# Kernel optimization log

Measured on AMD Instinct MI355X. Metric: run time of the kernel, lower is better.

Reference implementation:

```python
import jax, jax.numpy as jnp
import numpy as np

_N = 2048          # matrix_size (A_sparse.shape[0] in the original)
_NNZ = 32768       # number of factor / pred entries
_LOGCOND_EPS = 1e-12


def setup_inputs() -> dict:
    key = jax.random.key(0)
    k1, k2, k3, k4, k5 = jax.random.split(key, 5)
    pred_values = jax.random.normal(k1, (_NNZ,), dtype=jnp.float32)
    active_scales = jax.random.uniform(k2, (_NNZ,), dtype=jnp.float32) * 0.05
    A_factor = jax.random.normal(k3, (_N, _N), dtype=jnp.float32)
    factor_rows = jax.random.randint(k4, (_NNZ,), 0, _N, dtype=jnp.int32)
    factor_cols = jax.random.randint(k5, (_NNZ,), 0, _N, dtype=jnp.int32)
    return {
        "pred_values": pred_values,
        "active_scales": active_scales,
        "A_factor": A_factor,
        "factor_rows": factor_rows,
        "factor_cols": factor_cols,
    }


def reference(pred_values, active_scales, A_factor, factor_rows, factor_cols):
    n = A_factor.shape[0]
    dt = pred_values.dtype
    # SPD system matrix A (stands in for the original fixed A_sparse)
    A = A_factor @ A_factor.T / jnp.asarray(n, dt) + jnp.eye(n, dtype=dt)
    # Sparse factor L assembled from predicted values (scatter-add, dup-safe),
    # unit diagonal keeps L A L^T well conditioned / SPD.
    L = jnp.eye(n, dtype=dt).at[factor_rows, factor_cols].add(pred_values * active_scales)
    # Preconditioned matrix M = L A L^T (symmetric PSD)
    M = L @ A @ L.T
    M = 0.5 * (M + M.T)
    evals = jnp.linalg.eigvalsh(M)  # ascending
    lam_min = jnp.maximum(evals[0], _LOGCOND_EPS)
    lam_max = jnp.maximum(evals[-1], _LOGCOND_EPS)
    # loss = log(lambda_max) - log(lambda_min) = log condition number
    return jnp.log(lam_max) - jnp.log(lam_min)
```

## Files before the change

kernel.cpp:

```cpp
#include <hip/hip_runtime.h>

#define N2 2048
#define NNZ 32768
#define LK 22
#define NBL 128
#define BINCAP 64

typedef __attribute__((ext_vector_type(8))) _Float16 half8;
typedef __attribute__((ext_vector_type(4))) float f32x4;

#define AGENT __HIP_MEMORY_SCOPE_AGENT
#define AS1C(p) ((const __attribute__((address_space(1))) unsigned int*)(p))
#define AS3(p)  ((__attribute__((address_space(3))) unsigned int*)(p))

__device__ __forceinline__ unsigned short f2h(float f) {
  _Float16 h = (_Float16)f;
  return *(unsigned short*)&h;
}
__device__ __forceinline__ float h2f(unsigned short u) {
  _Float16 h = *(_Float16*)&u;
  return (float)h;
}

__global__ __launch_bounds__(256) void convert_kernel(const float* __restrict__ W,
                                                      unsigned short* __restrict__ Hf,
                                                      unsigned* __restrict__ cnt) {
  if (blockIdx.x < 8) cnt[blockIdx.x * 256 + threadIdx.x] = 0;
  int i4 = blockIdx.x * 256 + threadIdx.x;
  float4 w = ((const float4*)W)[i4];
  ushort4 h;
  h.x = f2h(w.x); h.y = f2h(w.y); h.z = f2h(w.z); h.w = f2h(w.w);
  ((ushort4*)Hf)[i4] = h;
}

__global__ __launch_bounds__(512) void gemm_f16_kernel(const unsigned short* __restrict__ Hf,
                                                       unsigned short* __restrict__ Ah,
                                                       const float* __restrict__ pred,
                                                       const float* __restrict__ scal,
                                                       const int* __restrict__ rows,
                                                       const int* __restrict__ cols,
                                                       unsigned* __restrict__ cnt,
                                                       int* __restrict__ bcol,
                                                       float* __restrict__ bval) {
  const int tid = threadIdx.x;
  if (blockIdx.x < 64) {
    int k = blockIdx.x * 512 + tid;
    int r = rows[k];
    unsigned pos = atomicAdd(&cnt[r], 1u);
    if (pos < BINCAP) {
      bcol[r * BINCAP + pos] = cols[k];
      bval[r * BINCAP + pos] = pred[k] * scal[k];
    }
  }

  __shared__ unsigned short Xs[2][64 * 32];
  __shared__ unsigned short Ys[2][128 * 32];
  __shared__ float Cred[64 * 132];
  const int w = tid >> 6, lane = tid & 63;
  const int half = w >> 2, wq = w & 3;
  const int swz = ((blockIdx.x & 7) << 6) | (blockIdx.x >> 3);
  const int bi = swz >> 4, bj = swz & 15;
  const int row0 = bi * 64, col0 = bj * 128;
  const int m0 = (wq & 1) * 32, n0 = (wq >> 1) * 64;
  f32x4 acc[2][4];
#pragma unroll
  for (int a = 0; a < 2; ++a)
#pragma unroll
    for (int b = 0; b < 4; ++b) acc[a][b] = (f32x4){0.f, 0.f, 0.f, 0.f};
  const int mrow = lane & 15, kseg = (lane >> 4) * 8;
  const int srowX = wq * 16 + (lane >> 2);
  const int srowY = wq * 32 + (lane >> 2);
  const int scol = (lane & 3) * 8;
  const int kbase = half * 1024;

  for (int k0 = 0; k0 < 1024; k0 += 32) {
    __syncthreads();
    __builtin_amdgcn_global_load_lds(
        AS1C(Hf + (size_t)(row0 + srowX) * 2048 + kbase + k0 + scol),
        AS3(Xs[half] + (wq * 16) * 32), 16, 0, 0);
#pragma unroll
    for (int q = 0; q < 2; ++q) {
      __builtin_amdgcn_global_load_lds(
          AS1C(Hf + (size_t)(col0 + srowY + q * 16) * 2048 + kbase + k0 + scol),
          AS3(Ys[half] + (wq * 32 + q * 16) * 32), 16, 0, 0);
    }
    __syncthreads();
    half8 af[2], bf[4];
#pragma unroll
    for (int t = 0; t < 2; ++t)
      af[t] = *(const half8*)(Xs[half] + (m0 + t * 16 + mrow) * 32 + kseg);
#pragma unroll
    for (int t = 0; t < 4; ++t)
      bf[t] = *(const half8*)(Ys[half] + (n0 + t * 16 + mrow) * 32 + kseg);
#pragma unroll
    for (int mt = 0; mt < 2; ++mt)
#pragma unroll
      for (int nt = 0; nt < 4; ++nt)
        acc[mt][nt] = __builtin_amdgcn_mfma_f32_16x16x32_f16(af[mt], bf[nt], acc[mt][nt], 0, 0, 0);
  }
  const int crow = (lane >> 4) * 4, ccol = lane & 15;
  __syncthreads();
  if (half == 1) {
#pragma unroll
    for (int mt = 0; mt < 2; ++mt)
#pragma unroll
      for (int nt = 0; nt < 4; ++nt)
#pragma unroll
        for (int r = 0; r < 4; ++r)
          Cred[(m0 + mt * 16 + crow + r) * 132 + n0 + nt * 16 + ccol] = acc[mt][nt][r];
  }
  __syncthreads();
  if (half == 0) {
    const float invn = 1.0f / 2048.0f;
#pragma unroll
    for (int mt = 0; mt < 2; ++mt)
#pragma unroll
      for (int nt = 0; nt < 4; ++nt) {
        const int gi0 = row0 + m0 + mt * 16 + crow;
        const int gj = col0 + n0 + nt * 16 + ccol;
        size_t base = (size_t)gi0 * 2048 + gj;
#pragma unroll
        for (int r = 0; r < 4; ++r) {
          float v = acc[mt][nt][r] +
                    Cred[(m0 + mt * 16 + crow + r) * 132 + n0 + nt * 16 + ccol];
          Ah[base + (size_t)r * 2048] = f2h(v * invn + ((gi0 + r == gj) ? 1.0f : 0.0f));
        }
      }
  }
}

__global__ __launch_bounds__(256) void gatherF_kernel(const unsigned* __restrict__ cnt,
                                                      const int* __restrict__ bcol,
                                                      const float* __restrict__ bval,
                                                      const unsigned short* __restrict__ Ah,
                                                      unsigned short* __restrict__ F) {
  const int r = blockIdx.x, tid = threadIdx.x;
  __shared__ int scol_[BINCAP];
  __shared__ float sval_[BINCAP];
  const unsigned ne = min(cnt[r], (unsigned)BINCAP);
  if (tid < ne) {
    scol_[tid] = bcol[r * BINCAP + tid];
    sval_[tid] = bval[r * BINCAP + tid];
  }
  __syncthreads();
  float acc[8] = {0.f, 0.f, 0.f, 0.f, 0.f, 0.f, 0.f, 0.f};
  unsigned e = 0;
  for (; e + 4 <= ne; e += 4) {
    uint4 q0 = *(const uint4*)(Ah + (size_t)scol_[e + 0] * 2048 + tid * 8);
    uint4 q1 = *(const uint4*)(Ah + (size_t)scol_[e + 1] * 2048 + tid * 8);
    uint4 q2 = *(const uint4*)(Ah + (size_t)scol_[e + 2] * 2048 + tid * 8);
    uint4 q3 = *(const uint4*)(Ah + (size_t)scol_[e + 3] * 2048 + tid * 8);
    half8 h0 = *(half8*)&q0, h1 = *(half8*)&q1, h2 = *(half8*)&q2, h3 = *(half8*)&q3;
    const float v0 = sval_[e], v1 = sval_[e + 1], v2 = sval_[e + 2], v3 = sval_[e + 3];
#pragma unroll
    for (int k = 0; k < 8; ++k) {
      acc[k] += v0 * (float)h0[k];
      acc[k] += v1 * (float)h1[k];
      acc[k] += v2 * (float)h2[k];
      acc[k] += v3 * (float)h3[k];
    }
  }
  for (; e < ne; ++e) {
    uint4 q = *(const uint4*)(Ah + (size_t)scol_[e] * 2048 + tid * 8);
    half8 hv = *(half8*)&q;
    const float v = sval_[e];
#pragma unroll
    for (int k = 0; k < 8; ++k) acc[k] += v * (float)hv[k];
  }
  unsigned short o[8];
#pragma unroll
  for (int k = 0; k < 8; ++k) o[k] = f2h(acc[k]);
  *(uint4*)(F + (size_t)r * 2048 + tid * 8) = *(uint4*)o;
}

__global__ __launch_bounds__(256) void transpose_kernel(const unsigned short* __restrict__ F,
                                                        unsigned short* __restrict__ Ft) {
  __shared__ unsigned short T2[64][66];
  const int bi = blockIdx.x, bj = blockIdx.y;
  const int c8 = (threadIdx.x & 7) * 8;
  const int rr = threadIdx.x >> 3;
#pragma unroll
  for (int h = 0; h < 2; ++h) {
    const int r = rr + h * 32;
    uint4 raw = *(const uint4*)(F + (size_t)(bj * 64 + r) * 2048 + bi * 64 + c8);
    const unsigned* pw = (const unsigned*)&raw;
#pragma unroll
    for (int i = 0; i < 4; ++i)
      *(unsigned*)&T2[r][c8 + i * 2] = pw[i];
  }
  __syncthreads();
#pragma unroll
  for (int h = 0; h < 2; ++h) {
    const int r = rr + h * 32;
    unsigned short tv[8];
#pragma unroll
    for (int k = 0; k < 8; ++k) tv[k] = T2[c8 + k][r];
    *(uint4*)(Ft + (size_t)(bi * 64 + r) * 2048 + bj * 64 + c8) = *(uint4*)tv;
  }
}

__global__ __launch_bounds__(256) void finalM_kernel(const unsigned* __restrict__ cnt,
                                                     const int* __restrict__ bcol,
                                                     const float* __restrict__ bval,
                                                     const unsigned short* __restrict__ Ah,
                                                     const unsigned short* __restrict__ F,
                                                     const unsigned short* __restrict__ Ft,
                                                     float* __restrict__ M) {
  const int r = blockIdx.x, tid = threadIdx.x;
  __shared__ int scol_[BINCAP];
  __shared__ float sval_[BINCAP];
  const unsigned ne = min(cnt[r], (unsigned)BINCAP);
  if (tid < ne) {
    scol_[tid] = bcol[r * BINCAP + tid];
    sval_[tid] = bval[r * BINCAP + tid];
  }
  __syncthreads();
  float acc[8] = {0.f, 0.f, 0.f, 0.f, 0.f, 0.f, 0.f, 0.f};
  unsigned e = 0;
  for (; e + 4 <= ne; e += 4) {
    uint4 q0 = *(const uint4*)(Ft + (size_t)scol_[e + 0] * 2048 + tid * 8);
    uint4 q1 = *(const uint4*)(Ft + (size_t)scol_[e + 1] * 2048 + tid * 8);
    uint4 q2 = *(const uint4*)(Ft + (size_t)scol_[e + 2] * 2048 + tid * 8);
    uint4 q3 = *(const uint4*)(Ft + (size_t)scol_[e + 3] * 2048 + tid * 8);
    half8 h0 = *(half8*)&q0, h1 = *(half8*)&q1, h2 = *(half8*)&q2, h3 = *(half8*)&q3;
    const float v0 = sval_[e], v1 = sval_[e + 1], v2 = sval_[e + 2], v3 = sval_[e + 3];
#pragma unroll
    for (int k = 0; k < 8; ++k) {
      acc[k] += v0 * (float)h0[k];
      acc[k] += v1 * (float)h1[k];
      acc[k] += v2 * (float)h2[k];
      acc[k] += v3 * (float)h3[k];
    }
  }
  for (; e < ne; ++e) {
    uint4 q = *(const uint4*)(Ft + (size_t)scol_[e] * 2048 + tid * 8);
    half8 hv = *(half8*)&q;
    const float v = sval_[e];
#pragma unroll
    for (int k = 0; k < 8; ++k) acc[k] += v * (float)hv[k];
  }
  const size_t off = (size_t)r * 2048 + tid * 8;
  uint4 ra = *(const uint4*)(Ah + off);
  uint4 rf = *(const uint4*)(F + off);
  uint4 rt = *(const uint4*)(Ft + off);
  half8 ha = *(half8*)&ra, hf = *(half8*)&rf, ht = *(half8*)&rt;
  float out[8];
#pragma unroll
  for (int k = 0; k < 8; ++k)
    out[k] = (float)ha[k] + ((float)hf[k] + (float)ht[k]) + acc[k];
  float4* Mo = (float4*)(M + off);
  Mo[0] = (float4){out[0], out[1], out[2], out[3]};
  Mo[1] = (float4){out[4], out[5], out[6], out[7]};
}

__device__ __forceinline__ float block_sum8(float v, float* red) {
#pragma unroll
  for (int off = 32; off; off >>= 1) v += __shfl_down(v, off);
  if ((threadIdx.x & 63) == 0) red[threadIdx.x >> 6] = v;
  __syncthreads();
  float r = ((red[0] + red[1]) + (red[2] + red[3])) +
            ((red[4] + red[5]) + (red[6] + red[7]));
  __syncthreads();
  return r;
}

__global__ __launch_bounds__(512) void lanczos_kernel(const float* __restrict__ M,
                                                      unsigned long long* __restrict__ Z0,
                                                      unsigned long long* __restrict__ Z1,
                                                      float* __restrict__ out) {
  const int tid = threadIdx.x, b = blockIdx.x;
  const int wave = tid >> 6, lane = tid & 63;
  __shared__ __align__(16) float Mlds[16 * 2048];
  __shared__ __align__(16) float VA[2048];
  __shared__ __align__(16) float VB[2048];
  __shared__ float red[8];
  __shared__ float al[LK + 2], b2[LK + 2];
  __shared__ float bnds[2], res[2];

  const float* Mblk = M + (size_t)b * 16 * 2048;
#pragma unroll
  for (int q = 0; q < 16; ++q)
    __builtin_amdgcn_global_load_lds(AS1C(Mblk + wave * 4096 + q * 256 + lane * 4),
                                     AS3(Mlds + wave * 4096 + q * 256), 16, 0, 0);

  float pv[4];
  float part = 0.f;
#pragma unroll
  for (int t = 0; t < 4; ++t) {
    int i = t * 512 + tid;
    unsigned u = (unsigned)i * 2654435761u;
    u ^= u >> 16; u *= 2246822519u; u ^= u >> 13;
    float rv = (float)(u >> 8) * (2.f / 16777216.f) - 1.f;
    pv[t] = rv;
    part += rv * rv;
  }
  float nrm = block_sum8(part, red);
  float innm = rsqrtf(nrm);
#pragma unroll
  for (int t = 0; t < 4; ++t) {
    int i = t * 512 + tid;
    VA[i] = pv[t] * innm;
    VB[i] = 0.f;
  }
  __syncthreads();

  float* Vcur = VA;
  float* Vprev = VB;
  float beta_prev = 0.f;

  for (int j = 1; j <= LK; ++j) {
    unsigned long long* Z = (j & 1) ? Z0 : Z1;
#pragma unroll
    for (int rr = 0; rr < 2; ++rr) {
      const int r = b * 16 + wave * 2 + rr;
      const float4* Mr = (const float4*)(Mlds + (wave * 2 + rr) * 2048);
      float s = 0.f;
#pragma unroll
      for (int t = 0; t < 8; ++t) {
        int idx = t * 64 + lane;
        float4 m4 = Mr[idx];
        float4 v4 = ((const float4*)Vcur)[idx];
        s += m4.x * v4.x + m4.y * v4.y + m4.z * v4.z + m4.w * v4.w;
      }
#pragma unroll
      for (int off = 32; off; off >>= 1) s += __shfl_down(s, off);
      if (lane == 0) {
        float zv = s - beta_prev * Vprev[r];
        unsigned long long pk = ((unsigned long long)(unsigned)j << 32) |
                                (unsigned long long)(unsigned)__float_as_uint(zv);
        __hip_atomic_store(&Z[r], pk, __ATOMIC_RELAXED, AGENT);
      }
    }

    float va[4];
#pragma unroll
    for (int t = 0; t < 4; ++t) va[t] = Vcur[t * 512 + tid];

    unsigned long long w4[4];
    int rounds = 0;
    for (;;) {
      bool ok = true;
#pragma unroll
      for (int t = 0; t < 4; ++t) {
        w4[t] = __hip_atomic_load(&Z[t * 512 + tid], __ATOMIC_RELAXED, AGENT);
        ok &= ((unsigned)(w4[t] >> 32) == (unsigned)j);
      }
      if (ok) break;
      if (rounds == 1)      __builtin_amdgcn_s_sleep(1);
      else if (rounds == 2) __builtin_amdgcn_s_sleep(2);
      else if (rounds >= 3) __builtin_amdgcn_s_sleep(8);
      ++rounds;
    }
    float za[4];
    float pa = 0.f;
#pragma unroll
    for (int t = 0; t < 4; ++t) {
      za[t] = __uint_as_float((unsigned)w4[t]);
      pa += za[t] * va[t];
    }
    float alpha = block_sum8(pa, red);
    float pb = 0.f;
#pragma unroll
    for (int t = 0; t < 4; ++t) {
      float rsd = za[t] - alpha * va[t];
      pb += rsd * rsd;
    }
    float beta2 = block_sum8(pb, red);
    float beta = sqrtf(fmaxf(beta2, 1e-30f));
    float invb = 1.f / beta;
    if (tid == 0) { al[j] = alpha; b2[j] = beta2; }
#pragma unroll
    for (int t = 0; t < 4; ++t) {
      int i = t * 512 + tid;
      Vprev[i] = (za[t] - alpha * va[t]) * invb;
    }
    float* tmp = Vprev; Vprev = Vcur; Vcur = tmp;
    beta_prev = beta;
    __syncthreads();
  }

  if (b == 0) {
    if (tid == 0) {
      float lo = 1e30f, hi = -1e30f;
      for (int i = 1; i <= LK; ++i) {
        float bl = (i > 1) ? sqrtf(b2[i - 1]) : 0.f;
        float br = (i < LK) ? sqrtf(b2[i]) : 0.f;
        lo = fminf(lo, al[i] - bl - br);
        hi = fmaxf(hi, al[i] + bl + br);
      }
      bnds[0] = lo; bnds[1] = hi;
    }
    __syncthreads();
    if (wave < 2) {
      const int tcount = (wave == 0) ? 1 : LK;
      float lo = bnds[0], hi = bnds[1];
      for (int round = 0; round < 4; ++round) {
        float x = lo + (hi - lo) * (float)(lane + 1) * (1.f / 65.f);
        int cnt = 0;
        float d = al[1] - x;
        if (fabsf(d) < 1e-25f) d = -1e-25f;
        if (d < 0.f) cnt++;
        for (int i = 2; i <= LK; ++i) {
          d = (al[i] - x) - b2[i - 1] / d;
          if (fabsf(d) < 1e-25f) d = -1e-25f;
          if (d < 0.f) cnt++;
        }
        bool ab = (cnt >= tcount);
        float cand_hi = ab ? x : hi;
        float cand_lo = ab ? lo : x;
#pragma unroll
        for (int off = 32; off; off >>= 1) {
          cand_hi = fminf(cand_hi, __shfl_down(cand_hi, off));
          cand_lo = fmaxf(cand_lo, __shfl_down(cand_lo, off));
        }
        cand_hi = __shfl(cand_hi, 0);
        cand_lo = __shfl(cand_lo, 0);
        hi = cand_hi;
        lo = fminf(cand_lo, hi);
      }
      if (lane == 0) res[wave] = 0.5f * (lo + hi);
    }
    __syncthreads();
    if (tid == 0) {
      float lmin = fmaxf(res[0], 1e-12f);
      float lmax = fmaxf(res[1], 1e-12f);
      out[0] = logf(lmax) - logf(lmin);
    }
  }
}

extern "C" void kernel_launch(void* const* d_in, const int* in_sizes, int n_in,
                              void* d_out, int out_size, void* d_ws, size_t ws_size,
                              hipStream_t stream) {
  const float* pred = (const float*)d_in[0];
  const float* scal = (const float*)d_in[1];
  const float* W    = (const float*)d_in[2];
  const int*   rows = (const int*)d_in[3];
  const int*   cols = (const int*)d_in[4];
  float* out = (float*)d_out;

  char* ws = (char*)d_ws;
  const size_t MB = 1024 * 1024;
  unsigned short* Hf = (unsigned short*)(ws);
  unsigned short* Ah = (unsigned short*)(ws + 8 * MB);
  unsigned short* F  = (unsigned short*)(ws + 16 * MB);
  unsigned short* Ft = (unsigned short*)(ws);
  float* M = (float*)(ws + 24 * MB);
  char* ctrl = ws + 40 * MB;
  unsigned* cnt  = (unsigned*)(ctrl);
  int*      bcol = (int*)(ctrl + 8192);
  float*    bval = (float*)(ctrl + 8192 + 524288);
  unsigned long long* Z0 = (unsigned long long*)(ctrl + 8192 + 1048576);
  unsigned long long* Z1 = (unsigned long long*)(ctrl + 8192 + 1048576 + 16384);

  convert_kernel<<<4096, 256, 0, stream>>>(W, Hf, cnt);
  gemm_f16_kernel<<<512, 512, 0, stream>>>(Hf, Ah, pred, scal, rows, cols, cnt, bcol, bval);

  gatherF_kernel<<<2048, 256, 0, stream>>>(cnt, bcol, bval, Ah, F);
  transpose_kernel<<<dim3(32, 32), 256, 0, stream>>>(F, Ft);
  finalM_kernel<<<2048, 256, 0, stream>>>(cnt, bcol, bval, Ah, F, Ft, M);

  lanczos_kernel<<<NBL, 512, 0, stream>>>(M, Z0, Z1, out);
}
```

Measured before the change: 256.5 us.

## Exploit symmetry of A: compute lower-triangle GEMM tiles and mirror-store transposes

The W·W^T GEMM now launches only the 272 tiles on or below the diagonal (in 128-column block units) instead of all 512. Each off-diagonal tile writes its result and also writes the transposed tile through shared memory, which roughly halves the GEMM arithmetic. The cost is an extra barrier and transposed store per block, fewer blocks to spread across the CUs, and a small serial loop to decode the tile index. The bcol/bval binning in blocks below 64 still runs because the block count stays above 64.

```diff
diff --git a/kernel.cpp b/kernel.cpp
--- a/kernel.cpp
+++ b/kernel.cpp
@@ -53,13 +53,24 @@
     }
   }
 
+  int bi, bj;
+  bool diag;
+  if (blockIdx.x < 32) {
+    bi = blockIdx.x; bj = bi >> 1; diag = true;
+  } else {
+    int idx = blockIdx.x - 32;
+    int j = 0;
+    while (j < 14 && idx >= (j + 1) * (30 - j)) ++j;
+    bj = j;
+    bi = 2 * j + 2 + (idx - j * (31 - j));
+    diag = false;
+  }
+
   __shared__ unsigned short Xs[2][64 * 32];
   __shared__ unsigned short Ys[2][128 * 32];
   __shared__ float Cred[64 * 132];
   const int w = tid >> 6, lane = tid & 63;
   const int half = w >> 2, wq = w & 3;
-  const int swz = ((blockIdx.x & 7) << 6) | (blockIdx.x >> 3);
-  const int bi = swz >> 4, bj = swz & 15;
   const int row0 = bi * 64, col0 = bj * 128;
   const int m0 = (wq & 1) * 32, n0 = (wq >> 1) * 64;
   f32x4 acc[2][4];
@@ -121,11 +132,25 @@
         size_t base = (size_t)gi0 * 2048 + gj;
 #pragma unroll
         for (int r = 0; r < 4; ++r) {
-          float v = acc[mt][nt][r] +
-                    Cred[(m0 + mt * 16 + crow + r) * 132 + n0 + nt * 16 + ccol];
-          Ah[base + (size_t)r * 2048] = f2h(v * invn + ((gi0 + r == gj) ? 1.0f : 0.0f));
+          const int li = (m0 + mt * 16 + crow + r) * 132 + n0 + nt * 16 + ccol;
+          float val = (acc[mt][nt][r] + Cred[li]) * invn +
+                      ((gi0 + r == gj) ? 1.0f : 0.0f);
+          Ah[base + (size_t)r * 2048] = f2h(val);
+          if (!diag) Cred[li] = val;
         }
       }
+  }
+  if (!diag) {
+    __syncthreads();
+    const int orow = tid >> 2;
+    const int cseg = (tid & 3) * 16;
+    unsigned short mv[16];
+#pragma unroll
+    for (int k = 0; k < 16; ++k)
+      mv[k] = f2h(Cred[(cseg + k) * 132 + orow]);
+    uint4* dst = (uint4*)(Ah + (size_t)(col0 + orow) * 2048 + row0 + cseg);
+    dst[0] = *(uint4*)&mv[0];
+    dst[1] = *(uint4*)&mv[8];
   }
 }
 
@@ -454,7 +479,7 @@
   unsigned long long* Z1 = (unsigned long long*)(ctrl + 8192 + 1048576 + 16384);
 
   convert_kernel<<<4096, 256, 0, stream>>>(W, Hf, cnt);
-  gemm_f16_kernel<<<512, 512, 0, stream>>>(Hf, Ah, pred, scal, rows, cols, cnt, bcol, bval);
+  gemm_f16_kernel<<<272, 512, 0, stream>>>(Hf, Ah, pred, scal, rows, cols, cnt, bcol, bval);
 
   gatherF_kernel<<<2048, 256, 0, stream>>>(cnt, bcol, bval, Ah, F);
   transpose_kernel<<<dim3(32, 32), 256, 0, stream>>>(F, Ft);
```

Result: no change. 255.4 us (-0.4%).
